# Kernel tuning notes

Measured on AMD Instinct MI355X. Metric: run time of the kernel, lower is better.

Reference implementation:

```python
import jax, jax.numpy as jnp
import numpy as np

B, TX, TS = 64, 2048, 10
D, L, NMELS, MAXR, R = 256, 1024, 80, 20, 2


def gru_cell(x, h, wih, whh, bih, bhh):
    # torch GRUCell: gates ordered (r, z, n)
    gi = x @ wih.T + bih
    gh = h @ whh.T + bhh
    ir, iz, inn = jnp.split(gi, 3, axis=-1)
    hr, hz, hn = jnp.split(gh, 3, axis=-1)
    r = jax.nn.sigmoid(ir + hr)
    z = jax.nn.sigmoid(iz + hz)
    n = jnp.tanh(inn + r * hn)
    return (1.0 - z) * n + z * h


def lstm_cell(x, h, c, wih, whh, bih, bhh):
    # torch LSTMCell: gates ordered (i, f, g, o)
    g = x @ wih.T + bih + h @ whh.T + bhh
    i, f, gg, o = jnp.split(g, 4, axis=-1)
    c_new = jax.nn.sigmoid(f) * c + jax.nn.sigmoid(i) * jnp.tanh(gg)
    h_new = jax.nn.sigmoid(o) * jnp.tanh(c_new)
    return h_new, c_new


def attention(enc, query, W, v):
    # u = v @ tanh(enc + W q); softmax over time
    qp = query @ W.T                                  # [B, D]
    u = jnp.tanh(enc + qp[:, None, :]) @ v            # [B, T]
    scores = jax.nn.softmax(u, axis=-1)               # [B, T]
    ctx = jnp.einsum('bt,btd->bd', scores, enc)       # [B, D]
    return scores, ctx


def setup_inputs() -> dict:
    key = jax.random.key(0)
    ks = jax.random.split(key, 40)
    n = lambda i, shape, s=0.02: jax.random.normal(ks[i], shape, dtype=jnp.float32) * s
    return {
        'encoder_seq': n(0, (B, TX, D), 1.0),
        'style_embed': n(1, (B, TS, D), 1.0),
        'prenet_in': n(2, (B, NMELS), 1.0),
        'h_text': n(3, (B, D), 1.0), 'h_style': n(4, (B, D), 1.0), 'h_attn': n(5, (B, D), 1.0),
        'h_r1': n(6, (B, L), 1.0), 'h_r2': n(7, (B, L), 1.0),
        'c_r1': n(8, (B, L), 1.0), 'c_r2': n(9, (B, L), 1.0),
        'cv_text': n(10, (B, D), 1.0), 'cv_style': n(11, (B, D), 1.0), 'cv': n(12, (B, D), 1.0),
        'fc1_w': n(13, (256, NMELS)), 'fc1_b': jnp.zeros((256,), jnp.float32),
        'fc2_w': n(14, (128, 256)), 'fc2_b': jnp.zeros((128,), jnp.float32),
        'tW': n(15, (D, D)), 'tv': n(16, (D,)),
        'sW': n(17, (D, D)), 'sv': n(18, (D,)),
        't_wih': n(19, (3 * D, D + 128)), 't_whh': n(20, (3 * D, D)),
        't_bih': jnp.zeros((3 * D,), jnp.float32), 't_bhh': jnp.zeros((3 * D,), jnp.float32),
        's_wih': n(21, (3 * D, D + 128)), 's_whh': n(22, (3 * D, D)),
        's_bih': jnp.zeros((3 * D,), jnp.float32), 's_bhh': jnp.zeros((3 * D,), jnp.float32),
        'a_wih': n(23, (3 * D, D + 128)), 'a_whh': n(24, (3 * D, D)),
        'a_bih': jnp.zeros((3 * D,), jnp.float32), 'a_bhh': jnp.zeros((3 * D,), jnp.float32),
        'ri_w': n(25, (L, 2 * D)), 'ri_b': jnp.zeros((L,), jnp.float32),
        'l1_wih': n(26, (4 * L, L)), 'l1_whh': n(27, (4 * L, L)),
        'l1_bih': jnp.zeros((4 * L,), jnp.float32), 'l1_bhh': jnp.zeros((4 * L,), jnp.float32),
        'l2_wih': n(28, (4 * L, L)), 'l2_whh': n(29, (4 * L, L)),
        'l2_bih': jnp.zeros((4 * L,), jnp.float32), 'l2_bhh': jnp.zeros((4 * L,), jnp.float32),
        'mp_w': n(30, (NMELS * MAXR, L)),
        't': 0,
    }


def reference(encoder_seq, style_embed, prenet_in, h_text, h_style, h_attn,
              h_r1, h_r2, c_r1, c_r2, cv_text, cv_style, cv,
              fc1_w, fc1_b, fc2_w, fc2_b, tW, tv, sW, sv,
              t_wih, t_whh, t_bih, t_bhh, s_wih, s_whh, s_bih, s_bhh,
              a_wih, a_whh, a_bih, a_bhh, ri_w, ri_b,
              l1_wih, l1_whh, l1_bih, l1_bhh, l2_wih, l2_whh, l2_bih, l2_bhh,
              mp_w, t):
    # PreNet (eval mode: no dropout)
    p = jax.nn.relu(prenet_in @ fc1_w.T + fc1_b)
    p = jax.nn.relu(p @ fc2_w.T + fc2_b)                      # [B, 128]

    text_in = jnp.concatenate([cv_text, p], axis=-1)          # [B, D+128]
    style_in = jnp.concatenate([cv_style, p], axis=-1)
    attn_in = jnp.concatenate([cv, p], axis=-1)

    h_text = gru_cell(text_in, h_text, t_wih, t_whh, t_bih, t_bhh)
    text_scores, cv_text = attention(encoder_seq, h_text, tW, tv)

    h_style = gru_cell(style_in, h_style, s_wih, s_whh, s_bih, s_bhh)
    style_scores, cv_style = attention(style_embed, h_style, sW, sv)

    cv_new = cv_text                                          # context_vec = text_context_vec
    h_attn = gru_cell(attn_in, h_attn, a_wih, a_whh, a_bih, a_bhh)

    x = jnp.concatenate([cv_new, h_attn], axis=1) @ ri_w.T + ri_b  # [B, L]
    h_r1, c_r1 = lstm_cell(x, h_r1, c_r1, l1_wih, l1_whh, l1_bih, l1_bhh)
    x = x + h_r1
    h_r2, c_r2 = lstm_cell(x, h_r2, c_r2, l2_wih, l2_whh, l2_bih, l2_bhh)
    x = x + h_r2

    mels = (x @ mp_w.T).reshape(B, NMELS, MAXR)[:, :, :R]     # [B, n_mels, r]
    return mels
```

## Files before the change

### kernel.cpp

```cpp
#include <hip/hip_runtime.h>
#include <hip/hip_bf16.h>

typedef unsigned short u16;
typedef unsigned int   u32;
typedef __attribute__((ext_vector_type(8))) short bf16x8;
typedef __attribute__((ext_vector_type(4))) float f32x4;

#define NB   64
#define NTX  2048
#define ND   256
#define NL   1024

#if __has_builtin(__builtin_amdgcn_exp2f)
#define EXP2F(x) __builtin_amdgcn_exp2f(x)
#else
#define EXP2F(x) exp2f(x)
#endif
#if __has_builtin(__builtin_amdgcn_rcpf)
#define RCPF(x) __builtin_amdgcn_rcpf(x)
#else
#define RCPF(x) (1.0f/(x))
#endif

__device__ __forceinline__ u16 f2bf(float f){
  union { float f; u32 u; } c; c.f = f;
  return (u16)((c.u + 0x7fffu + ((c.u >> 16) & 1u)) >> 16);
}
__device__ __forceinline__ u32 pk2(float a, float b){
  return (u32)f2bf(a) | ((u32)f2bf(b) << 16);
}
__device__ __forceinline__ float sigmf(float x){ return 1.f/(1.f+__expf(-x)); }
__device__ __forceinline__ float tanhf_fast(float x){
  x = fminf(fmaxf(x, -15.f), 15.f);
  float e = __expf(2.f*x);
  return (e - 1.f) / (e + 1.f);
}
__device__ __forceinline__ float dot_rowf(const float* __restrict__ row,
                                          const float* __restrict__ x, int K4){
  float acc = 0.f;
  for (int j = 0; j < K4; ++j){
    float4 w = *(const float4*)(row + j*4);
    const float* xp = x + j*4;
    acc += w.x*xp[0] + w.y*xp[1] + w.z*xp[2] + w.w*xp[3];
  }
  return acc;
}

__global__ __launch_bounds__(256) void k_pre1(
    const float* __restrict__ cv_text, const float* __restrict__ cv,
    const float* __restrict__ h_text,  const float* __restrict__ h_attn,
    const float* __restrict__ prenet_in,
    const float* __restrict__ fc1_w, const float* __restrict__ fc1_b,
    const float* __restrict__ h_r1, const float* __restrict__ h_r2,
    float* __restrict__ xtext, float* __restrict__ xattn,
    float* __restrict__ htT,  float* __restrict__ haT,
    float* __restrict__ p1T,
    u16* __restrict__ hb1, u16* __restrict__ hb2)
{
  __shared__ float ld[64][65];
  const int blk = blockIdx.x, tid = threadIdx.x;
  if (blk < 16){
    int a = blk >> 2; int c0 = (blk & 3)*64;
    const float* src = (a==0)?cv_text:(a==1)?cv:(a==2)?h_text:h_attn;
    float* dst = (a==0)?xtext:(a==1)?xattn:(a==2)?htT:haT;
    const int r = tid >> 2, q = tid & 3;
    #pragma unroll
    for (int i = 0; i < 4; ++i){
      float4 v = *(const float4*)(src + (size_t)r*256 + c0 + q*16 + i*4);
      ld[r][q*16+i*4+0] = v.x; ld[r][q*16+i*4+1] = v.y;
      ld[r][q*16+i*4+2] = v.z; ld[r][q*16+i*4+3] = v.w;
    }
    __syncthreads();
    const int cc = tid >> 2;
    #pragma unroll
    for (int i = 0; i < 4; ++i){
      int b0 = q*16 + i*4;
      float4 o = { ld[b0+0][cc], ld[b0+1][cc], ld[b0+2][cc], ld[b0+3][cc] };
      *(float4*)(dst + (size_t)(c0+cc)*64 + b0) = o;
    }
  } else if (blk < 80){
    const int wave = tid >> 6, lane = tid & 63;
    const int n = (blk - 16)*4 + wave;
    float acc = fc1_b[n];
    const float* wr = fc1_w + (size_t)n*80;
    const float* xr = prenet_in + (size_t)lane*80;
    #pragma unroll
    for (int k = 0; k < 80; k += 4){
      float4 w = *(const float4*)(wr + k);
      acc += w.x*xr[k] + w.y*xr[k+1] + w.z*xr[k+2] + w.w*xr[k+3];
    }
    p1T[n*64 + lane] = fmaxf(acc, 0.f);
  } else {
    const int t2 = blk - 80;
    const float* src = (t2 < 32) ? h_r1 : h_r2;
    u16* dst = (t2 < 32) ? hb1 : hb2;
    const int base = (t2 & 31)*2048 + tid*8;
    float4 a = *(const float4*)(src + base);
    float4 b = *(const float4*)(src + base + 4);
    uint4 o = { pk2(a.x,a.y), pk2(a.z,a.w), pk2(b.x,b.y), pk2(b.z,b.w) };
    *(uint4*)(dst + base) = o;
  }
}

__global__ __launch_bounds__(256) void k_pre2(
    const float* __restrict__ p1T,
    const float* __restrict__ fc2_w, const float* __restrict__ fc2_b,
    float* __restrict__ xtext, float* __restrict__ xattn)
{
  const int tid = threadIdx.x, w = tid >> 6, lane = tid & 63;
  const int n = blockIdx.x;
  __shared__ float red[4][64];
  float acc = 0.f;
  const float* wr = fc2_w + (size_t)n*256 + w*64;
  const float* xb = p1T + w*64*64 + lane;
  #pragma unroll
  for (int k = 0; k < 64; k += 4){
    float4 wv = *(const float4*)(wr + k);
    acc += wv.x*xb[(k+0)*64] + wv.y*xb[(k+1)*64]
         + wv.z*xb[(k+2)*64] + wv.w*xb[(k+3)*64];
  }
  red[w][lane] = acc;
  __syncthreads();
  if (w == 0){
    float v = fmaxf(red[0][lane]+red[1][lane]+red[2][lane]+red[3][lane] + fc2_b[n], 0.f);
    xtext[(size_t)(256+n)*64 + lane] = v;
    xattn[(size_t)(256+n)*64 + lane] = v;
  }
}

__global__ __launch_bounds__(512) void k_gru(
    const float* __restrict__ t_wih, const float* __restrict__ t_whh,
    const float* __restrict__ t_bih, const float* __restrict__ t_bhh,
    const float* __restrict__ a_wih, const float* __restrict__ a_whh,
    const float* __restrict__ a_bih, const float* __restrict__ a_bhh,
    const float* __restrict__ xtext, const float* __restrict__ xattn,
    const float* __restrict__ htT,  const float* __restrict__ haT,
    float* __restrict__ htnT, u16* __restrict__ xrib)
{
  const int tid = threadIdx.x, w = tid >> 6, lane = tid & 63;
  const int isA = blockIdx.x >= 256;
  const int d = blockIdx.x & 255;
  const float* wih = isA ? a_wih : t_wih;
  const float* whh = isA ? a_whh : t_whh;
  const float* xT  = isA ? xattn : xtext;
  const float* hT  = isA ? haT   : htT;
  __shared__ float red[8][6][64];
  float s0=0.f,s1=0.f,s2=0.f,s3=0.f,s4=0.f,s5=0.f;
  {
    const float* wr = wih + (size_t)d*384       + w*48;
    const float* wz = wih + (size_t)(256+d)*384 + w*48;
    const float* wn = wih + (size_t)(512+d)*384 + w*48;
    const float* xb = xT + w*48*64 + lane;
    #pragma unroll 4
    for (int k = 0; k < 48; k += 4){
      float4 ar = *(const float4*)(wr + k);
      float4 az = *(const float4*)(wz + k);
      float4 an = *(const float4*)(wn + k);
      float x0 = xb[(k+0)*64], x1 = xb[(k+1)*64];
      float x2 = xb[(k+2)*64], x3 = xb[(k+3)*64];
      s0 += ar.x*x0 + ar.y*x1 + ar.z*x2 + ar.w*x3;
      s1 += az.x*x0 + az.y*x1 + az.z*x2 + az.w*x3;
      s2 += an.x*x0 + an.y*x1 + an.z*x2 + an.w*x3;
    }
  }
  {
    const float* vr = whh + (size_t)d*256       + w*32;
    const float* vz = whh + (size_t)(256+d)*256 + w*32;
    const float* vn = whh + (size_t)(512+d)*256 + w*32;
    const float* hb = hT + w*32*64 + lane;
    #pragma unroll 4
    for (int k = 0; k < 32; k += 4){
      float4 ar = *(const float4*)(vr + k);
      float4 az = *(const float4*)(vz + k);
      float4 an = *(const float4*)(vn + k);
      float h0 = hb[(k+0)*64], h1 = hb[(k+1)*64];
      float h2 = hb[(k+2)*64], h3 = hb[(k+3)*64];
      s3 += ar.x*h0 + ar.y*h1 + ar.z*h2 + ar.w*h3;
      s4 += az.x*h0 + az.y*h1 + az.z*h2 + az.w*h3;
      s5 += an.x*h0 + an.y*h1 + an.z*h2 + an.w*h3;
    }
  }
  red[w][0][lane]=s0; red[w][1][lane]=s1; red[w][2][lane]=s2;
  red[w][3][lane]=s3; red[w][4][lane]=s4; red[w][5][lane]=s5;
  __syncthreads();
  if (w == 0){
    const float* bih = isA ? a_bih : t_bih;
    const float* bhh = isA ? a_bhh : t_bhh;
    float g6[6];
    #pragma unroll
    for (int i = 0; i < 6; ++i){
      float a = 0.f;
      #pragma unroll
      for (int ww = 0; ww < 8; ++ww) a += red[ww][i][lane];
      g6[i] = a;
    }
    float gir = bih[d]     + g6[0];
    float giz = bih[256+d] + g6[1];
    float gin = bih[512+d] + g6[2];
    float ghr = bhh[d]     + g6[3];
    float ghz = bhh[256+d] + g6[4];
    float ghn = bhh[512+d] + g6[5];
    float hd = hT[d*64 + lane];
    float r  = sigmf(gir + ghr), z = sigmf(giz + ghz);
    float nn = tanhf_fast(gin + r*ghn);
    float hnew = (1.f - z)*nn + z*hd;
    if (isA) xrib[(size_t)lane*512 + 256 + d] = f2bf(hnew);
    else     htnT[(size_t)d*64 + lane]        = hnew;
  }
}

__global__ __launch_bounds__(256) void k_qp(
    const float* __restrict__ tWm, const float* __restrict__ htnT,
    float* __restrict__ qp)
{
  const int tid = threadIdx.x, w = tid >> 6, lane = tid & 63;
  const int d = blockIdx.x;
  __shared__ float red[4][64];
  float acc = 0.f;
  const float* wr = tWm + (size_t)d*256 + w*64;
  const float* xb = htnT + w*64*64 + lane;
  #pragma unroll
  for (int k = 0; k < 64; k += 4){
    float4 wv = *(const float4*)(wr + k);
    acc += wv.x*xb[(k+0)*64] + wv.y*xb[(k+1)*64]
         + wv.z*xb[(k+2)*64] + wv.w*xb[(k+3)*64];
  }
  red[w][lane] = acc;
  __syncthreads();
  if (w == 0)
    qp[lane*ND + d] = red[0][lane]+red[1][lane]+red[2][lane]+red[3][lane];
}

__global__ __launch_bounds__(256) void k_attn_part(
    const float* __restrict__ enc, const float* __restrict__ qp,
    const float* __restrict__ tv,  float* __restrict__ attnP)
{
  const int tid = threadIdx.x, b = blockIdx.x, ch = blockIdx.y;
  const int wave = tid >> 6, lane = tid & 63;
  const float C2  = 2.885390082f;
  const float L2E = 1.4426950408f;
  __shared__ float qpL[256], vL[256], ctxL[4][256], sL[4];
  qpL[tid] = qp[b*ND + tid] * C2;
  vL[tid]  = tv[tid] * 2.f;
  __syncthreads();

  const float q0 = qpL[lane*4+0], q1 = qpL[lane*4+1], q2 = qpL[lane*4+2], q3 = qpL[lane*4+3];
  const float v0 = vL[lane*4+0],  v1 = vL[lane*4+1],  v2 = vL[lane*4+2],  v3 = vL[lane*4+3];
  float vs = 0.5f*(v0 + v1 + v2 + v3);
  #pragma unroll
  for (int off = 1; off < 64; off <<= 1) vs += __shfl_xor(vs, off);
  const float VS = vs;

  float cx0=0.f, cx1=0.f, cx2=0.f, cx3=0.f, sacc=0.f;
  const float* base = enc + ((size_t)b*NTX + (size_t)ch*128 + wave*32)*ND + lane*4;
  #pragma unroll 4
  for (int i = 0; i < 32; ++i){
    float4 ev = *(const float4*)(base + (size_t)i*ND);
    float e0 = ev.x, e1 = ev.y, e2 = ev.z, e3 = ev.w;
    float srow;
    {
      float u0 = EXP2F(__builtin_fmaf(e0, C2, q0));
      float u1 = EXP2F(__builtin_fmaf(e1, C2, q1));
      float u2 = EXP2F(__builtin_fmaf(e2, C2, q2));
      float u3 = EXP2F(__builtin_fmaf(e3, C2, q3));
      srow = v0*RCPF(u0 + 1.f) + v1*RCPF(u1 + 1.f)
           + v2*RCPF(u2 + 1.f) + v3*RCPF(u3 + 1.f);
    }
    #pragma unroll
    for (int off = 1; off < 64; off <<= 1) srow += __shfl_xor(srow, off);
    float w = EXP2F((VS - srow) * L2E);
    sacc += w;
    cx0 = __builtin_fmaf(w, e0, cx0); cx1 = __builtin_fmaf(w, e1, cx1);
    cx2 = __builtin_fmaf(w, e2, cx2); cx3 = __builtin_fmaf(w, e3, cx3);
  }
  ctxL[wave][lane*4+0]=cx0; ctxL[wave][lane*4+1]=cx1;
  ctxL[wave][lane*4+2]=cx2; ctxL[wave][lane*4+3]=cx3;
  if (lane == 0) sL[wave] = sacc;
  __syncthreads();
  float c = ctxL[0][tid]+ctxL[1][tid]+ctxL[2][tid]+ctxL[3][tid];
  float* dst = attnP + ((size_t)b*16 + ch)*257;
  dst[tid] = c;
  if (tid == 0) dst[256] = sL[0]+sL[1]+sL[2]+sL[3];
}

__global__ __launch_bounds__(256) void k_attn_red(
    const float* __restrict__ attnP, u16* __restrict__ xrib)
{
  const int tid = threadIdx.x, b = blockIdx.x;
  float c = 0.f, s = 0.f;
  for (int ch = 0; ch < 16; ++ch){
    const float* src = attnP + ((size_t)b*16 + ch)*257;
    c += src[tid]; s += src[256];
  }
  xrib[(size_t)b*512 + tid] = f2bf(c / s);
}


__global__ __launch_bounds__(512) void k_mm_ri(
    const u16* __restrict__ xrib, const float* __restrict__ ri_w,
    const float* __restrict__ ri_b, float* __restrict__ x0,
    u16* __restrict__ x0b)
{
  __shared__ float Rs[8][4][4][65];
  const int tid = threadIdx.x, lane = tid & 63, w = tid >> 6;
  const int n0 = blockIdx.x * 16;
  f32x4 acc[4];
  #pragma unroll
  for (int i = 0; i < 4; ++i) acc[i] = (f32x4){0.f,0.f,0.f,0.f};
  const int kbase = w*64;
  const float* wr = ri_w + (size_t)(n0 + (lane & 15))*512 + kbase + (lane >> 4)*8;
  const u16* xs = xrib + (size_t)(lane & 15)*512 + kbase + (lane >> 4)*8;
  #pragma unroll
  for (int t = 0; t < 2; ++t){
    float4 wa = *(const float4*)(wr + t*32);
    float4 wb = *(const float4*)(wr + t*32 + 4);
    union { bf16x8 v; uint4 u; } bf;
    bf.u.x = pk2(wa.x,wa.y); bf.u.y = pk2(wa.z,wa.w);
    bf.u.z = pk2(wb.x,wb.y); bf.u.w = pk2(wb.z,wb.w);
    #pragma unroll
    for (int fb = 0; fb < 4; ++fb){
      union { bf16x8 v; uint4 u; } af;
      af.u = *(const uint4*)(xs + fb*16*512 + t*32);
      acc[fb] = __builtin_amdgcn_mfma_f32_16x16x32_bf16(af.v, bf.v, acc[fb], 0, 0, 0);
    }
  }
  #pragma unroll
  for (int fb = 0; fb < 4; ++fb)
    #pragma unroll
    for (int r = 0; r < 4; ++r) Rs[w][fb][r][lane] = acc[fb][r];
  __syncthreads();
  if (tid < 256){
    const int b = tid >> 2, c4 = (tid & 3)*4;
    const int fb = b >> 4, q = (b >> 2) & 3, reg = b & 3;
    #pragma unroll
    for (int cc = 0; cc < 4; ++cc){
      const int c = c4 + cc;
      float v = ri_b[n0 + c];
      #pragma unroll
      for (int ww = 0; ww < 8; ++ww) v += Rs[ww][fb][reg][q*16 + c];
      x0[(size_t)b*1024 + n0 + c]  = v;
      x0b[(size_t)b*1024 + n0 + c] = f2bf(v);
    }
  }
}

__global__ __launch_bounds__(1024) void k_lstm(
    const float* __restrict__ Wih, const float* __restrict__ Whh,
    const u16* __restrict__ xb, const u16* __restrict__ hb,
    const float* __restrict__ bih, const float* __restrict__ bhh,
    const float* __restrict__ c_in,
    const float* __restrict__ xin, float* __restrict__ xout,
    u16* __restrict__ xoutb)
{
  __shared__ float Rs[16][4][4][65];
  const int tid = threadIdx.x, lane = tid & 63, w = tid >> 6;
  const int j0 = blockIdx.x * 4;
  const float* W = (w < 8) ? Wih : Whh;
  const u16*   X = (w < 8) ? xb  : hb;
  const int kbase = (w & 7) * 128;

  f32x4 acc[4];
  #pragma unroll
  for (int i = 0; i < 4; ++i) acc[i] = (f32x4){0.f,0.f,0.f,0.f};
  const int r16 = lane & 15;
  const int g = r16 >> 2, jq = r16 & 3;
  const float* wr = W + (size_t)(g*1024 + j0 + jq)*1024 + kbase + (lane >> 4)*8;
  #pragma unroll
  for (int t = 0; t < 4; ++t){
    float4 wa = *(const float4*)(wr + t*32);
    float4 wb = *(const float4*)(wr + t*32 + 4);
    union { bf16x8 v; uint4 u; } bf;
    bf.u.x = pk2(wa.x,wa.y); bf.u.y = pk2(wa.z,wa.w);
    bf.u.z = pk2(wb.x,wb.y); bf.u.w = pk2(wb.z,wb.w);
    #pragma unroll
    for (int fb = 0; fb < 4; ++fb){
      union { bf16x8 v; uint4 u; } af;
      af.u = *(const uint4*)(X + (size_t)(fb*16 + r16)*1024 + kbase + (lane >> 4)*8 + t*32);
      acc[fb] = __builtin_amdgcn_mfma_f32_16x16x32_bf16(af.v, bf.v, acc[fb], 0, 0, 0);
    }
  }
  #pragma unroll
  for (int fb = 0; fb < 4; ++fb)
    #pragma unroll
    for (int r = 0; r < 4; ++r) Rs[w][fb][r][lane] = acc[fb][r];
  __syncthreads();

  if (tid < 256){
    const int b  = tid >> 2, jq2 = tid & 3;
    const int j  = j0 + jq2;
    const int fb = b >> 4, q = (b >> 2) & 3, reg = b & 3;
    float gate[4];
    #pragma unroll
    for (int gg = 0; gg < 4; ++gg){
      const int li = q*16 + gg*4 + jq2;
      float a = bih[gg*1024 + j] + bhh[gg*1024 + j];
      #pragma unroll
      for (int ww = 0; ww < 16; ++ww) a += Rs[ww][fb][reg][li];
      gate[gg] = a;
    }
    float ii = sigmf(gate[0]), ff = sigmf(gate[1]);
    float gv = tanhf_fast(gate[2]), oo = sigmf(gate[3]);
    float cc = ff * c_in[(size_t)b*1024 + j] + ii * gv;
    float hh = oo * tanhf_fast(cc);
    float xo = xin[(size_t)b*1024 + j] + hh;
    xout[(size_t)b*1024 + j]  = xo;
    xoutb[(size_t)b*1024 + j] = f2bf(xo);
  }
}

__global__ __launch_bounds__(256) void k_mels(
    const float* __restrict__ x2, const float* __restrict__ mp_w,
    float* __restrict__ out)
{
  const int tid = threadIdx.x, b = blockIdx.x;
  __shared__ float xL[NL];
  #pragma unroll
  for (int i = 0; i < 4; ++i){
    int j = tid + 256*i;
    xL[j] = x2[(size_t)b*NL + j];
  }
  __syncthreads();
  if (tid < 160){
    int m = tid >> 1, r = tid & 1;
    float acc = dot_rowf(mp_w + (size_t)(m*20 + r)*NL, xL, 256);
    out[b*160 + tid] = acc;
  }
}

extern "C" void kernel_launch(void* const* d_in, const int* in_sizes, int n_in,
                              void* d_out, int out_size, void* d_ws, size_t ws_size,
                              hipStream_t stream)
{
  (void)in_sizes; (void)n_in; (void)out_size; (void)ws_size;
  const float* enc     = (const float*)d_in[0];
  const float* pre_in  = (const float*)d_in[2];
  const float* h_text  = (const float*)d_in[3];
  const float* h_attn  = (const float*)d_in[5];
  const float* h_r1    = (const float*)d_in[6];
  const float* h_r2    = (const float*)d_in[7];
  const float* c_r1    = (const float*)d_in[8];
  const float* c_r2    = (const float*)d_in[9];
  const float* cv_text = (const float*)d_in[10];
  const float* cv      = (const float*)d_in[12];
  const float* fc1_w   = (const float*)d_in[13];
  const float* fc1_b   = (const float*)d_in[14];
  const float* fc2_w   = (const float*)d_in[15];
  const float* fc2_b   = (const float*)d_in[16];
  const float* tWm     = (const float*)d_in[17];
  const float* tv      = (const float*)d_in[18];
  const float* t_wih   = (const float*)d_in[21];
  const float* t_whh   = (const float*)d_in[22];
  const float* t_bih   = (const float*)d_in[23];
  const float* t_bhh   = (const float*)d_in[24];
  const float* a_wih   = (const float*)d_in[29];
  const float* a_whh   = (const float*)d_in[30];
  const float* a_bih   = (const float*)d_in[31];
  const float* a_bhh   = (const float*)d_in[32];
  const float* ri_w    = (const float*)d_in[33];
  const float* ri_b    = (const float*)d_in[34];
  const float* l1_wih  = (const float*)d_in[35];
  const float* l1_whh  = (const float*)d_in[36];
  const float* l1_bih  = (const float*)d_in[37];
  const float* l1_bhh  = (const float*)d_in[38];
  const float* l2_wih  = (const float*)d_in[39];
  const float* l2_whh  = (const float*)d_in[40];
  const float* l2_bih  = (const float*)d_in[41];
  const float* l2_bhh  = (const float*)d_in[42];
  const float* mp_w    = (const float*)d_in[43];

  float* ws    = (float*)d_ws;
  float* qp    = ws;
  float* attnP = qp    + 16384;
  float* x0    = attnP + 263168;
  float* x1    = x0    + 65536;
  float* x2    = x1    + 65536;
  float* xtext = x2    + 65536;
  float* xattn = xtext + 24576;
  float* htT   = xattn + 24576;
  float* haT   = htT   + 16384;
  float* htnT  = haT   + 16384;
  float* p1T   = htnT  + 16384;
  u16*   hb1   = (u16*)(p1T + 16384);
  u16*   hb2   = hb1 + 65536;
  u16*   xrib  = hb2 + 65536;
  u16*   x0b   = xrib + 32768;
  u16*   x1b   = x0b + 65536;
  u16*   x2b   = x1b + 65536;

  k_pre1<<<144, 256, 0, stream>>>(cv_text, cv, h_text, h_attn,
      pre_in, fc1_w, fc1_b, h_r1, h_r2,
      xtext, xattn, htT, haT, p1T, hb1, hb2);
  k_pre2<<<128, 256, 0, stream>>>(p1T, fc2_w, fc2_b, xtext, xattn);
  k_gru<<<512, 512, 0, stream>>>(t_wih, t_whh, t_bih, t_bhh,
      a_wih, a_whh, a_bih, a_bhh, xtext, xattn, htT, haT, htnT, xrib);
  k_qp<<<256, 256, 0, stream>>>(tWm, htnT, qp);

  k_attn_part<<<dim3(64,16), 256, 0, stream>>>(enc, qp, tv, attnP);
  k_attn_red<<<64, 256, 0, stream>>>(attnP, xrib);

  k_mm_ri<<<64, 512, 0, stream>>>(xrib, ri_w, ri_b, x0, x0b);

  k_lstm<<<256, 1024, 0, stream>>>(l1_wih, l1_whh, x0b, hb1,
      l1_bih, l1_bhh, c_r1, x0, x1, x1b);
  k_lstm<<<256, 1024, 0, stream>>>(l2_wih, l2_whh, x1b, hb2,
      l2_bih, l2_bhh, c_r2, x1, x2, x2b);

  k_mels<<<64, 256, 0, stream>>>(x2, mp_w, (float*)d_out);
}
```

Measured before the change: 115.6 us.

## Fuse all decoder stages into one cooperative persistent kernel with grid syncs

Replaces the chain of ten small kernel launches with a single cooperative kernel of 256 blocks × 1024 threads. Stages are separated by grid.sync() and mapped onto virtual sub-blocks. The point is to remove launch gaps and per-kernel ramp-up on a tiny, latency-bound step. It also reshapes the attention split (fewer partials, the attnP workspace shrinks) and folds the context normalization into the ri matmul stage, and it skews the shared-memory reduction indices to avoid bank conflicts. In exchange, every stage now runs at a fixed 1024-thread occupancy, and each grid barrier has its own cost.

```diff
diff --git a/kernel.cpp b/kernel.cpp
--- a/kernel.cpp
+++ b/kernel.cpp
@@ -1,5 +1,8 @@
 #include <hip/hip_runtime.h>
+#include <hip/hip_cooperative_groups.h>
 #include <hip/hip_bf16.h>
+
+namespace cg = cooperative_groups;
 
 typedef unsigned short u16;
 typedef unsigned int   u32;
@@ -35,330 +38,32 @@
   float e = __expf(2.f*x);
   return (e - 1.f) / (e + 1.f);
 }
-__device__ __forceinline__ float dot_rowf(const float* __restrict__ row,
-                                          const float* __restrict__ x, int K4){
-  float acc = 0.f;
-  for (int j = 0; j < K4; ++j){
-    float4 w = *(const float4*)(row + j*4);
-    const float* xp = x + j*4;
-    acc += w.x*xp[0] + w.y*xp[1] + w.z*xp[2] + w.w*xp[3];
-  }
-  return acc;
-}
-
-__global__ __launch_bounds__(256) void k_pre1(
-    const float* __restrict__ cv_text, const float* __restrict__ cv,
-    const float* __restrict__ h_text,  const float* __restrict__ h_attn,
-    const float* __restrict__ prenet_in,
-    const float* __restrict__ fc1_w, const float* __restrict__ fc1_b,
-    const float* __restrict__ h_r1, const float* __restrict__ h_r2,
-    float* __restrict__ xtext, float* __restrict__ xattn,
-    float* __restrict__ htT,  float* __restrict__ haT,
-    float* __restrict__ p1T,
-    u16* __restrict__ hb1, u16* __restrict__ hb2)
-{
-  __shared__ float ld[64][65];
-  const int blk = blockIdx.x, tid = threadIdx.x;
-  if (blk < 16){
-    int a = blk >> 2; int c0 = (blk & 3)*64;
-    const float* src = (a==0)?cv_text:(a==1)?cv:(a==2)?h_text:h_attn;
-    float* dst = (a==0)?xtext:(a==1)?xattn:(a==2)?htT:haT;
-    const int r = tid >> 2, q = tid & 3;
-    #pragma unroll
-    for (int i = 0; i < 4; ++i){
-      float4 v = *(const float4*)(src + (size_t)r*256 + c0 + q*16 + i*4);
-      ld[r][q*16+i*4+0] = v.x; ld[r][q*16+i*4+1] = v.y;
-      ld[r][q*16+i*4+2] = v.z; ld[r][q*16+i*4+3] = v.w;
-    }
-    __syncthreads();
-    const int cc = tid >> 2;
-    #pragma unroll
-    for (int i = 0; i < 4; ++i){
-      int b0 = q*16 + i*4;
-      float4 o = { ld[b0+0][cc], ld[b0+1][cc], ld[b0+2][cc], ld[b0+3][cc] };
-      *(float4*)(dst + (size_t)(c0+cc)*64 + b0) = o;
-    }
-  } else if (blk < 80){
-    const int wave = tid >> 6, lane = tid & 63;
-    const int n = (blk - 16)*4 + wave;
-    float acc = fc1_b[n];
-    const float* wr = fc1_w + (size_t)n*80;
-    const float* xr = prenet_in + (size_t)lane*80;
-    #pragma unroll
-    for (int k = 0; k < 80; k += 4){
-      float4 w = *(const float4*)(wr + k);
-      acc += w.x*xr[k] + w.y*xr[k+1] + w.z*xr[k+2] + w.w*xr[k+3];
-    }
-    p1T[n*64 + lane] = fmaxf(acc, 0.f);
-  } else {
-    const int t2 = blk - 80;
-    const float* src = (t2 < 32) ? h_r1 : h_r2;
-    u16* dst = (t2 < 32) ? hb1 : hb2;
-    const int base = (t2 & 31)*2048 + tid*8;
-    float4 a = *(const float4*)(src + base);
-    float4 b = *(const float4*)(src + base + 4);
-    uint4 o = { pk2(a.x,a.y), pk2(a.z,a.w), pk2(b.x,b.y), pk2(b.z,b.w) };
-    *(uint4*)(dst + base) = o;
-  }
-}
-
-__global__ __launch_bounds__(256) void k_pre2(
-    const float* __restrict__ p1T,
-    const float* __restrict__ fc2_w, const float* __restrict__ fc2_b,
-    float* __restrict__ xtext, float* __restrict__ xattn)
-{
-  const int tid = threadIdx.x, w = tid >> 6, lane = tid & 63;
-  const int n = blockIdx.x;
-  __shared__ float red[4][64];
-  float acc = 0.f;
-  const float* wr = fc2_w + (size_t)n*256 + w*64;
-  const float* xb = p1T + w*64*64 + lane;
-  #pragma unroll
-  for (int k = 0; k < 64; k += 4){
-    float4 wv = *(const float4*)(wr + k);
-    acc += wv.x*xb[(k+0)*64] + wv.y*xb[(k+1)*64]
-         + wv.z*xb[(k+2)*64] + wv.w*xb[(k+3)*64];
-  }
-  red[w][lane] = acc;
-  __syncthreads();
-  if (w == 0){
-    float v = fmaxf(red[0][lane]+red[1][lane]+red[2][lane]+red[3][lane] + fc2_b[n], 0.f);
-    xtext[(size_t)(256+n)*64 + lane] = v;
-    xattn[(size_t)(256+n)*64 + lane] = v;
-  }
-}
-
-__global__ __launch_bounds__(512) void k_gru(
-    const float* __restrict__ t_wih, const float* __restrict__ t_whh,
-    const float* __restrict__ t_bih, const float* __restrict__ t_bhh,
-    const float* __restrict__ a_wih, const float* __restrict__ a_whh,
-    const float* __restrict__ a_bih, const float* __restrict__ a_bhh,
-    const float* __restrict__ xtext, const float* __restrict__ xattn,
-    const float* __restrict__ htT,  const float* __restrict__ haT,
-    float* __restrict__ htnT, u16* __restrict__ xrib)
-{
-  const int tid = threadIdx.x, w = tid >> 6, lane = tid & 63;
-  const int isA = blockIdx.x >= 256;
-  const int d = blockIdx.x & 255;
-  const float* wih = isA ? a_wih : t_wih;
-  const float* whh = isA ? a_whh : t_whh;
-  const float* xT  = isA ? xattn : xtext;
-  const float* hT  = isA ? haT   : htT;
-  __shared__ float red[8][6][64];
-  float s0=0.f,s1=0.f,s2=0.f,s3=0.f,s4=0.f,s5=0.f;
-  {
-    const float* wr = wih + (size_t)d*384       + w*48;
-    const float* wz = wih + (size_t)(256+d)*384 + w*48;
-    const float* wn = wih + (size_t)(512+d)*384 + w*48;
-    const float* xb = xT + w*48*64 + lane;
-    #pragma unroll 4
-    for (int k = 0; k < 48; k += 4){
-      float4 ar = *(const float4*)(wr + k);
-      float4 az = *(const float4*)(wz + k);
-      float4 an = *(const float4*)(wn + k);
-      float x0 = xb[(k+0)*64], x1 = xb[(k+1)*64];
-      float x2 = xb[(k+2)*64], x3 = xb[(k+3)*64];
-      s0 += ar.x*x0 + ar.y*x1 + ar.z*x2 + ar.w*x3;
-      s1 += az.x*x0 + az.y*x1 + az.z*x2 + az.w*x3;
-      s2 += an.x*x0 + an.y*x1 + an.z*x2 + an.w*x3;
-    }
-  }
-  {
-    const float* vr = whh + (size_t)d*256       + w*32;
-    const float* vz = whh + (size_t)(256+d)*256 + w*32;
-    const float* vn = whh + (size_t)(512+d)*256 + w*32;
-    const float* hb = hT + w*32*64 + lane;
-    #pragma unroll 4
-    for (int k = 0; k < 32; k += 4){
-      float4 ar = *(const float4*)(vr + k);
-      float4 az = *(const float4*)(vz + k);
-      float4 an = *(const float4*)(vn + k);
-      float h0 = hb[(k+0)*64], h1 = hb[(k+1)*64];
-      float h2 = hb[(k+2)*64], h3 = hb[(k+3)*64];
-      s3 += ar.x*h0 + ar.y*h1 + ar.z*h2 + ar.w*h3;
-      s4 += az.x*h0 + az.y*h1 + az.z*h2 + az.w*h3;
-      s5 += an.x*h0 + an.y*h1 + an.z*h2 + an.w*h3;
-    }
-  }
-  red[w][0][lane]=s0; red[w][1][lane]=s1; red[w][2][lane]=s2;
-  red[w][3][lane]=s3; red[w][4][lane]=s4; red[w][5][lane]=s5;
-  __syncthreads();
-  if (w == 0){
-    const float* bih = isA ? a_bih : t_bih;
-    const float* bhh = isA ? a_bhh : t_bhh;
-    float g6[6];
-    #pragma unroll
-    for (int i = 0; i < 6; ++i){
-      float a = 0.f;
-      #pragma unroll
-      for (int ww = 0; ww < 8; ++ww) a += red[ww][i][lane];
-      g6[i] = a;
-    }
-    float gir = bih[d]     + g6[0];
-    float giz = bih[256+d] + g6[1];
-    float gin = bih[512+d] + g6[2];
-    float ghr = bhh[d]     + g6[3];
-    float ghz = bhh[256+d] + g6[4];
-    float ghn = bhh[512+d] + g6[5];
-    float hd = hT[d*64 + lane];
-    float r  = sigmf(gir + ghr), z = sigmf(giz + ghz);
-    float nn = tanhf_fast(gin + r*ghn);
-    float hnew = (1.f - z)*nn + z*hd;
-    if (isA) xrib[(size_t)lane*512 + 256 + d] = f2bf(hnew);
-    else     htnT[(size_t)d*64 + lane]        = hnew;
-  }
-}
-
-__global__ __launch_bounds__(256) void k_qp(
-    const float* __restrict__ tWm, const float* __restrict__ htnT,
-    float* __restrict__ qp)
-{
-  const int tid = threadIdx.x, w = tid >> 6, lane = tid & 63;
-  const int d = blockIdx.x;
-  __shared__ float red[4][64];
-  float acc = 0.f;
-  const float* wr = tWm + (size_t)d*256 + w*64;
-  const float* xb = htnT + w*64*64 + lane;
-  #pragma unroll
-  for (int k = 0; k < 64; k += 4){
-    float4 wv = *(const float4*)(wr + k);
-    acc += wv.x*xb[(k+0)*64] + wv.y*xb[(k+1)*64]
-         + wv.z*xb[(k+2)*64] + wv.w*xb[(k+3)*64];
-  }
-  red[w][lane] = acc;
-  __syncthreads();
-  if (w == 0)
-    qp[lane*ND + d] = red[0][lane]+red[1][lane]+red[2][lane]+red[3][lane];
-}
-
-__global__ __launch_bounds__(256) void k_attn_part(
-    const float* __restrict__ enc, const float* __restrict__ qp,
-    const float* __restrict__ tv,  float* __restrict__ attnP)
-{
-  const int tid = threadIdx.x, b = blockIdx.x, ch = blockIdx.y;
-  const int wave = tid >> 6, lane = tid & 63;
-  const float C2  = 2.885390082f;
-  const float L2E = 1.4426950408f;
-  __shared__ float qpL[256], vL[256], ctxL[4][256], sL[4];
-  qpL[tid] = qp[b*ND + tid] * C2;
-  vL[tid]  = tv[tid] * 2.f;
-  __syncthreads();
-
-  const float q0 = qpL[lane*4+0], q1 = qpL[lane*4+1], q2 = qpL[lane*4+2], q3 = qpL[lane*4+3];
-  const float v0 = vL[lane*4+0],  v1 = vL[lane*4+1],  v2 = vL[lane*4+2],  v3 = vL[lane*4+3];
-  float vs = 0.5f*(v0 + v1 + v2 + v3);
-  #pragma unroll
-  for (int off = 1; off < 64; off <<= 1) vs += __shfl_xor(vs, off);
-  const float VS = vs;
-
-  float cx0=0.f, cx1=0.f, cx2=0.f, cx3=0.f, sacc=0.f;
-  const float* base = enc + ((size_t)b*NTX + (size_t)ch*128 + wave*32)*ND + lane*4;
-  #pragma unroll 4
-  for (int i = 0; i < 32; ++i){
-    float4 ev = *(const float4*)(base + (size_t)i*ND);
-    float e0 = ev.x, e1 = ev.y, e2 = ev.z, e3 = ev.w;
-    float srow;
-    {
-      float u0 = EXP2F(__builtin_fmaf(e0, C2, q0));
-      float u1 = EXP2F(__builtin_fmaf(e1, C2, q1));
-      float u2 = EXP2F(__builtin_fmaf(e2, C2, q2));
-      float u3 = EXP2F(__builtin_fmaf(e3, C2, q3));
-      srow = v0*RCPF(u0 + 1.f) + v1*RCPF(u1 + 1.f)
-           + v2*RCPF(u2 + 1.f) + v3*RCPF(u3 + 1.f);
-    }
-    #pragma unroll
-    for (int off = 1; off < 64; off <<= 1) srow += __shfl_xor(srow, off);
-    float w = EXP2F((VS - srow) * L2E);
-    sacc += w;
-    cx0 = __builtin_fmaf(w, e0, cx0); cx1 = __builtin_fmaf(w, e1, cx1);
-    cx2 = __builtin_fmaf(w, e2, cx2); cx3 = __builtin_fmaf(w, e3, cx3);
-  }
-  ctxL[wave][lane*4+0]=cx0; ctxL[wave][lane*4+1]=cx1;
-  ctxL[wave][lane*4+2]=cx2; ctxL[wave][lane*4+3]=cx3;
-  if (lane == 0) sL[wave] = sacc;
-  __syncthreads();
-  float c = ctxL[0][tid]+ctxL[1][tid]+ctxL[2][tid]+ctxL[3][tid];
-  float* dst = attnP + ((size_t)b*16 + ch)*257;
-  dst[tid] = c;
-  if (tid == 0) dst[256] = sL[0]+sL[1]+sL[2]+sL[3];
-}
-
-__global__ __launch_bounds__(256) void k_attn_red(
-    const float* __restrict__ attnP, u16* __restrict__ xrib)
-{
-  const int tid = threadIdx.x, b = blockIdx.x;
-  float c = 0.f, s = 0.f;
-  for (int ch = 0; ch < 16; ++ch){
-    const float* src = attnP + ((size_t)b*16 + ch)*257;
-    c += src[tid]; s += src[256];
-  }
-  xrib[(size_t)b*512 + tid] = f2bf(c / s);
-}
-
-
-__global__ __launch_bounds__(512) void k_mm_ri(
-    const u16* __restrict__ xrib, const float* __restrict__ ri_w,
-    const float* __restrict__ ri_b, float* __restrict__ x0,
-    u16* __restrict__ x0b)
-{
-  __shared__ float Rs[8][4][4][65];
-  const int tid = threadIdx.x, lane = tid & 63, w = tid >> 6;
-  const int n0 = blockIdx.x * 16;
-  f32x4 acc[4];
-  #pragma unroll
-  for (int i = 0; i < 4; ++i) acc[i] = (f32x4){0.f,0.f,0.f,0.f};
-  const int kbase = w*64;
-  const float* wr = ri_w + (size_t)(n0 + (lane & 15))*512 + kbase + (lane >> 4)*8;
-  const u16* xs = xrib + (size_t)(lane & 15)*512 + kbase + (lane >> 4)*8;
-  #pragma unroll
-  for (int t = 0; t < 2; ++t){
-    float4 wa = *(const float4*)(wr + t*32);
-    float4 wb = *(const float4*)(wr + t*32 + 4);
-    union { bf16x8 v; uint4 u; } bf;
-    bf.u.x = pk2(wa.x,wa.y); bf.u.y = pk2(wa.z,wa.w);
-    bf.u.z = pk2(wb.x,wb.y); bf.u.w = pk2(wb.z,wb.w);
-    #pragma unroll
-    for (int fb = 0; fb < 4; ++fb){
-      union { bf16x8 v; uint4 u; } af;
-      af.u = *(const uint4*)(xs + fb*16*512 + t*32);
-      acc[fb] = __builtin_amdgcn_mfma_f32_16x16x32_bf16(af.v, bf.v, acc[fb], 0, 0, 0);
-    }
-  }
-  #pragma unroll
-  for (int fb = 0; fb < 4; ++fb)
-    #pragma unroll
-    for (int r = 0; r < 4; ++r) Rs[w][fb][r][lane] = acc[fb][r];
-  __syncthreads();
-  if (tid < 256){
-    const int b = tid >> 2, c4 = (tid & 3)*4;
-    const int fb = b >> 4, q = (b >> 2) & 3, reg = b & 3;
-    #pragma unroll
-    for (int cc = 0; cc < 4; ++cc){
-      const int c = c4 + cc;
-      float v = ri_b[n0 + c];
-      #pragma unroll
-      for (int ww = 0; ww < 8; ++ww) v += Rs[ww][fb][reg][q*16 + c];
-      x0[(size_t)b*1024 + n0 + c]  = v;
-      x0b[(size_t)b*1024 + n0 + c] = f2bf(v);
-    }
-  }
-}
-
-__global__ __launch_bounds__(1024) void k_lstm(
+
+struct MA {
+  const float *enc, *pre_in, *h_r1, *h_r2, *c_r1, *c_r2,
+              *cv_text, *cv, *h_text, *h_attn,
+              *fc1_w, *fc1_b, *fc2_w, *fc2_b, *tWm, *tv,
+              *t_wih, *t_whh, *t_bih, *t_bhh,
+              *a_wih, *a_whh, *a_bih, *a_bhh,
+              *ri_w, *ri_b, *l1_wih, *l1_whh, *l1_bih, *l1_bhh,
+              *l2_wih, *l2_whh, *l2_bih, *l2_bhh, *mp_w;
+  float *qp, *attnP, *x0, *x1, *x2, *xtext, *xattn, *htT, *haT, *htnT, *p1T;
+  u16 *hb1, *hb2, *xrib, *x0b, *x1b, *x2b;
+  float* out;
+};
+
+__device__ __forceinline__ void lstm_stage(const MA& a, float* Rs,
     const float* __restrict__ Wih, const float* __restrict__ Whh,
     const u16* __restrict__ xb, const u16* __restrict__ hb,
     const float* __restrict__ bih, const float* __restrict__ bhh,
-    const float* __restrict__ c_in,
-    const float* __restrict__ xin, float* __restrict__ xout,
-    u16* __restrict__ xoutb)
+    const float* __restrict__ c_in, const float* __restrict__ xin,
+    float* __restrict__ xout, u16* __restrict__ xoutb)
 {
-  __shared__ float Rs[16][4][4][65];
   const int tid = threadIdx.x, lane = tid & 63, w = tid >> 6;
   const int j0 = blockIdx.x * 4;
   const float* W = (w < 8) ? Wih : Whh;
   const u16*   X = (w < 8) ? xb  : hb;
   const int kbase = (w & 7) * 128;
-
   f32x4 acc[4];
   #pragma unroll
   for (int i = 0; i < 4; ++i) acc[i] = (f32x4){0.f,0.f,0.f,0.f};
@@ -382,9 +87,9 @@
   #pragma unroll
   for (int fb = 0; fb < 4; ++fb)
     #pragma unroll
-    for (int r = 0; r < 4; ++r) Rs[w][fb][r][lane] = acc[fb][r];
+    for (int r = 0; r < 4; ++r)
+      Rs[w*1024 + fb*256 + r*64 + ((lane + w*4) & 63)] = acc[fb][r];
   __syncthreads();
-
   if (tid < 256){
     const int b  = tid >> 2, jq2 = tid & 3;
     const int j  = j0 + jq2;
@@ -393,10 +98,11 @@
     #pragma unroll
     for (int gg = 0; gg < 4; ++gg){
       const int li = q*16 + gg*4 + jq2;
-      float a = bih[gg*1024 + j] + bhh[gg*1024 + j];
-      #pragma unroll
-      for (int ww = 0; ww < 16; ++ww) a += Rs[ww][fb][reg][li];
-      gate[gg] = a;
+      float s = bih[gg*1024 + j] + bhh[gg*1024 + j];
+      #pragma unroll
+      for (int ww = 0; ww < 16; ++ww)
+        s += Rs[ww*1024 + fb*256 + reg*64 + ((li + ww*4) & 63)];
+      gate[gg] = s;
     }
     float ii = sigmf(gate[0]), ff = sigmf(gate[1]);
     float gv = tanhf_fast(gate[2]), oo = sigmf(gate[3]);
@@ -408,22 +114,318 @@
   }
 }
 
-__global__ __launch_bounds__(256) void k_mels(
-    const float* __restrict__ x2, const float* __restrict__ mp_w,
-    float* __restrict__ out)
+__global__ __launch_bounds__(1024) void k_mega(MA a)
 {
-  const int tid = threadIdx.x, b = blockIdx.x;
-  __shared__ float xL[NL];
-  #pragma unroll
-  for (int i = 0; i < 4; ++i){
-    int j = tid + 256*i;
-    xL[j] = x2[(size_t)b*NL + j];
-  }
-  __syncthreads();
-  if (tid < 160){
-    int m = tid >> 1, r = tid & 1;
-    float acc = dot_rowf(mp_w + (size_t)(m*20 + r)*NL, xL, 256);
-    out[b*160 + tid] = acc;
+  __shared__ char smem[65536];
+  float* smemf = (float*)smem;
+  cg::grid_group grid = cg::this_grid();
+  const int tid = threadIdx.x, blk = blockIdx.x;
+  const int lane = tid & 63, w = tid >> 6;
+  const int vblk = blk*4 + (tid >> 8), vtid = tid & 255;
+
+  if (vblk < 16){
+    int ai = vblk >> 2, c0 = (vblk & 3)*64;
+    const float* src = (ai==0)?a.cv_text:(ai==1)?a.cv:(ai==2)?a.h_text:a.h_attn;
+    float* dst = (ai==0)?a.xtext:(ai==1)?a.xattn:(ai==2)?a.htT:a.haT;
+    const int b = vtid & 63, cq = vtid >> 6;
+    #pragma unroll
+    for (int i = 0; i < 16; ++i){
+      int c = c0 + cq + i*4;
+      dst[(size_t)c*64 + b] = src[(size_t)b*256 + c];
+    }
+  } else if (vblk < 80){
+    const int wv = vtid >> 6, ln = vtid & 63;
+    const int n = (vblk - 16)*4 + wv;
+    float acc = a.fc1_b[n];
+    const float* wr = a.fc1_w + (size_t)n*80;
+    const float* xr = a.pre_in + (size_t)ln*80;
+    #pragma unroll
+    for (int k = 0; k < 80; k += 4){
+      float4 wq = *(const float4*)(wr + k);
+      acc += wq.x*xr[k] + wq.y*xr[k+1] + wq.z*xr[k+2] + wq.w*xr[k+3];
+    }
+    a.p1T[n*64 + ln] = fmaxf(acc, 0.f);
+  } else if (vblk < 144){
+    const int t2 = vblk - 80;
+    const float* src = (t2 < 32) ? a.h_r1 : a.h_r2;
+    u16* dst = (t2 < 32) ? a.hb1 : a.hb2;
+    const int base = (t2 & 31)*2048 + vtid*8;
+    float4 p = *(const float4*)(src + base);
+    float4 q = *(const float4*)(src + base + 4);
+    uint4 o = { pk2(p.x,p.y), pk2(p.z,p.w), pk2(q.x,q.y), pk2(q.z,q.w) };
+    *(uint4*)(dst + base) = o;
+  }
+  grid.sync();
+
+  if (blk < 32){
+    const int n = vblk;
+    const int wv = vtid >> 6, ln = vtid & 63;
+    float* red = smemf + (tid >> 8)*256;
+    float acc = 0.f;
+    const float* wr = a.fc2_w + (size_t)n*256 + wv*64;
+    const float* xb = a.p1T + wv*64*64 + ln;
+    #pragma unroll
+    for (int k = 0; k < 64; k += 4){
+      float4 wq = *(const float4*)(wr + k);
+      acc += wq.x*xb[(k+0)*64] + wq.y*xb[(k+1)*64]
+           + wq.z*xb[(k+2)*64] + wq.w*xb[(k+3)*64];
+    }
+    red[wv*64 + ln] = acc;
+    __syncthreads();
+    if (wv == 0){
+      float v = fmaxf(red[ln]+red[64+ln]+red[128+ln]+red[192+ln] + a.fc2_b[n], 0.f);
+      a.xtext[(size_t)(256+n)*64 + ln] = v;
+      a.xattn[(size_t)(256+n)*64 + ln] = v;
+    }
+  }
+  grid.sync();
+
+  {
+    const int d = blk;
+    const int isA = (w >= 8), w8 = w & 7;
+    const float* wih = isA ? a.a_wih : a.t_wih;
+    const float* whh = isA ? a.a_whh : a.t_whh;
+    const float* xT  = isA ? a.xattn : a.xtext;
+    const float* hT  = isA ? a.haT   : a.htT;
+    float* red = smemf;
+    float s0=0.f,s1=0.f,s2=0.f,s3=0.f,s4=0.f,s5=0.f;
+    {
+      const float* wr = wih + (size_t)d*384       + w8*48;
+      const float* wz = wih + (size_t)(256+d)*384 + w8*48;
+      const float* wn = wih + (size_t)(512+d)*384 + w8*48;
+      const float* xb = xT + w8*48*64 + lane;
+      #pragma unroll 4
+      for (int k = 0; k < 48; k += 4){
+        float4 ar = *(const float4*)(wr + k);
+        float4 az = *(const float4*)(wz + k);
+        float4 an = *(const float4*)(wn + k);
+        float x0 = xb[(k+0)*64], x1 = xb[(k+1)*64];
+        float x2 = xb[(k+2)*64], x3 = xb[(k+3)*64];
+        s0 += ar.x*x0 + ar.y*x1 + ar.z*x2 + ar.w*x3;
+        s1 += az.x*x0 + az.y*x1 + az.z*x2 + az.w*x3;
+        s2 += an.x*x0 + an.y*x1 + an.z*x2 + an.w*x3;
+      }
+    }
+    {
+      const float* vr = whh + (size_t)d*256       + w8*32;
+      const float* vz = whh + (size_t)(256+d)*256 + w8*32;
+      const float* vn = whh + (size_t)(512+d)*256 + w8*32;
+      const float* hb = hT + w8*32*64 + lane;
+      #pragma unroll 4
+      for (int k = 0; k < 32; k += 4){
+        float4 ar = *(const float4*)(vr + k);
+        float4 az = *(const float4*)(vz + k);
+        float4 an = *(const float4*)(vn + k);
+        float h0 = hb[(k+0)*64], h1 = hb[(k+1)*64];
+        float h2 = hb[(k+2)*64], h3 = hb[(k+3)*64];
+        s3 += ar.x*h0 + ar.y*h1 + ar.z*h2 + ar.w*h3;
+        s4 += az.x*h0 + az.y*h1 + az.z*h2 + az.w*h3;
+        s5 += an.x*h0 + an.y*h1 + an.z*h2 + an.w*h3;
+      }
+    }
+    red[(w*6+0)*64+lane]=s0; red[(w*6+1)*64+lane]=s1; red[(w*6+2)*64+lane]=s2;
+    red[(w*6+3)*64+lane]=s3; red[(w*6+4)*64+lane]=s4; red[(w*6+5)*64+lane]=s5;
+    __syncthreads();
+    if (w == 0 || w == 8){
+      const int base = (w == 8) ? 8 : 0;
+      const float* bih = (w==8) ? a.a_bih : a.t_bih;
+      const float* bhh = (w==8) ? a.a_bhh : a.t_bhh;
+      const float* hT2 = (w==8) ? a.haT   : a.htT;
+      float g6[6];
+      #pragma unroll
+      for (int i = 0; i < 6; ++i){
+        float s = 0.f;
+        #pragma unroll
+        for (int ww = 0; ww < 8; ++ww) s += red[((base+ww)*6+i)*64 + lane];
+        g6[i] = s;
+      }
+      float gir = bih[d]     + g6[0];
+      float giz = bih[256+d] + g6[1];
+      float gin = bih[512+d] + g6[2];
+      float ghr = bhh[d]     + g6[3];
+      float ghz = bhh[256+d] + g6[4];
+      float ghn = bhh[512+d] + g6[5];
+      float hd = hT2[d*64 + lane];
+      float r  = sigmf(gir + ghr), z = sigmf(giz + ghz);
+      float nn = tanhf_fast(gin + r*ghn);
+      float hnew = (1.f - z)*nn + z*hd;
+      if (w == 8) a.xrib[(size_t)lane*512 + 256 + d] = f2bf(hnew);
+      else        a.htnT[(size_t)d*64 + lane]        = hnew;
+    }
+  }
+  grid.sync();
+
+  if (blk < 64){
+    const int d = vblk;
+    const int wv = vtid >> 6, ln = vtid & 63;
+    float* red = smemf + (tid >> 8)*256;
+    float acc = 0.f;
+    const float* wr = a.tWm + (size_t)d*256 + wv*64;
+    const float* xb = a.htnT + wv*64*64 + ln;
+    #pragma unroll
+    for (int k = 0; k < 64; k += 4){
+      float4 wq = *(const float4*)(wr + k);
+      acc += wq.x*xb[(k+0)*64] + wq.y*xb[(k+1)*64]
+           + wq.z*xb[(k+2)*64] + wq.w*xb[(k+3)*64];
+    }
+    red[wv*64 + ln] = acc;
+    __syncthreads();
+    if (wv == 0)
+      a.qp[ln*ND + d] = red[ln]+red[64+ln]+red[128+ln]+red[192+ln];
+  }
+  grid.sync();
+
+  {
+    const int b = blk >> 2, chg = blk & 3;
+    const float C2  = 2.885390082f;
+    const float L2E = 1.4426950408f;
+    float* qpL  = smemf;
+    float* vL   = smemf + 256;
+    float* ctxL = smemf + 512;
+    float* sL   = smemf + 512 + 4096;
+    if (tid < 256){
+      qpL[tid] = a.qp[b*ND + tid] * C2;
+      vL[tid]  = a.tv[tid] * 2.f;
+    }
+    __syncthreads();
+    const float q0 = qpL[lane*4+0], q1 = qpL[lane*4+1], q2 = qpL[lane*4+2], q3 = qpL[lane*4+3];
+    const float v0 = vL[lane*4+0],  v1 = vL[lane*4+1],  v2 = vL[lane*4+2],  v3 = vL[lane*4+3];
+    float vs = 0.5f*(v0 + v1 + v2 + v3);
+    #pragma unroll
+    for (int off = 1; off < 64; off <<= 1) vs += __shfl_xor(vs, off);
+    const float VS = vs;
+    float cx0=0.f, cx1=0.f, cx2=0.f, cx3=0.f, sacc=0.f;
+    const float* base = a.enc + ((size_t)b*NTX + (size_t)chg*512 + w*32)*ND + lane*4;
+    #pragma unroll 4
+    for (int i = 0; i < 32; ++i){
+      float4 ev = *(const float4*)(base + (size_t)i*ND);
+      float e0 = ev.x, e1 = ev.y, e2 = ev.z, e3 = ev.w;
+      float u0 = EXP2F(__builtin_fmaf(e0, C2, q0));
+      float u1 = EXP2F(__builtin_fmaf(e1, C2, q1));
+      float u2 = EXP2F(__builtin_fmaf(e2, C2, q2));
+      float u3 = EXP2F(__builtin_fmaf(e3, C2, q3));
+      float srow = v0*RCPF(u0 + 1.f) + v1*RCPF(u1 + 1.f)
+                 + v2*RCPF(u2 + 1.f) + v3*RCPF(u3 + 1.f);
+      #pragma unroll
+      for (int off = 1; off < 64; off <<= 1) srow += __shfl_xor(srow, off);
+      float ww = EXP2F((VS - srow) * L2E);
+      sacc += ww;
+      cx0 = __builtin_fmaf(ww, e0, cx0); cx1 = __builtin_fmaf(ww, e1, cx1);
+      cx2 = __builtin_fmaf(ww, e2, cx2); cx3 = __builtin_fmaf(ww, e3, cx3);
+    }
+    ctxL[w*256 + lane*4+0]=cx0; ctxL[w*256 + lane*4+1]=cx1;
+    ctxL[w*256 + lane*4+2]=cx2; ctxL[w*256 + lane*4+3]=cx3;
+    if (lane == 0) sL[w] = sacc;
+    __syncthreads();
+    if (tid < 256){
+      float c = 0.f;
+      #pragma unroll
+      for (int ww = 0; ww < 16; ++ww) c += ctxL[ww*256 + tid];
+      a.attnP[(size_t)blk*257 + tid] = c;
+      if (tid == 0){
+        float s = 0.f;
+        #pragma unroll
+        for (int ww = 0; ww < 16; ++ww) s += sL[ww];
+        a.attnP[(size_t)blk*257 + 256] = s;
+      }
+    }
+  }
+  grid.sync();
+
+  if (blk < 64){
+    u16*   xctxb = (u16*)smem;
+    float* Rs    = (float*)(smem + 32768);
+    {
+      const int b = tid >> 4, cg16 = tid & 15;
+      float s = a.attnP[(size_t)(b*4+0)*257 + 256] + a.attnP[(size_t)(b*4+1)*257 + 256]
+              + a.attnP[(size_t)(b*4+2)*257 + 256] + a.attnP[(size_t)(b*4+3)*257 + 256];
+      float inv = RCPF(s);
+      #pragma unroll
+      for (int i = 0; i < 16; ++i){
+        int c = cg16*16 + i;
+        float v = a.attnP[(size_t)(b*4+0)*257 + c] + a.attnP[(size_t)(b*4+1)*257 + c]
+                + a.attnP[(size_t)(b*4+2)*257 + c] + a.attnP[(size_t)(b*4+3)*257 + c];
+        xctxb[b*256 + c] = f2bf(v * inv);
+      }
+    }
+    __syncthreads();
+    const int n0 = blk * 16;
+    if (w < 8){
+      f32x4 acc[4];
+      #pragma unroll
+      for (int i = 0; i < 4; ++i) acc[i] = (f32x4){0.f,0.f,0.f,0.f};
+      const int kbase = w*64;
+      const float* wr = a.ri_w + (size_t)(n0 + (lane & 15))*512 + kbase + (lane >> 4)*8;
+      #pragma unroll
+      for (int t = 0; t < 2; ++t){
+        float4 wa = *(const float4*)(wr + t*32);
+        float4 wb = *(const float4*)(wr + t*32 + 4);
+        union { bf16x8 v; uint4 u; } bf;
+        bf.u.x = pk2(wa.x,wa.y); bf.u.y = pk2(wa.z,wa.w);
+        bf.u.z = pk2(wb.x,wb.y); bf.u.w = pk2(wb.z,wb.w);
+        #pragma unroll
+        for (int fb = 0; fb < 4; ++fb){
+          union { bf16x8 v; uint4 u; } af;
+          const int row = fb*16 + (lane & 15);
+          if (w < 4)
+            af.u = *(const uint4*)(xctxb + row*256 + kbase + (lane >> 4)*8 + t*32);
+          else
+            af.u = *(const uint4*)(a.xrib + (size_t)row*512 + kbase + (lane >> 4)*8 + t*32);
+          acc[fb] = __builtin_amdgcn_mfma_f32_16x16x32_bf16(af.v, bf.v, acc[fb], 0, 0, 0);
+        }
+      }
+      #pragma unroll
+      for (int fb = 0; fb < 4; ++fb)
+        #pragma unroll
+        for (int r = 0; r < 4; ++r)
+          Rs[w*1024 + fb*256 + r*64 + ((lane + w*4) & 63)] = acc[fb][r];
+    }
+    __syncthreads();
+    if (tid < 256){
+      const int b = tid >> 2, c4 = (tid & 3)*4;
+      const int fb = b >> 4, q = (b >> 2) & 3, reg = b & 3;
+      #pragma unroll
+      for (int cc = 0; cc < 4; ++cc){
+        const int c = c4 + cc;
+        const int li = q*16 + c;
+        float v = a.ri_b[n0 + c];
+        #pragma unroll
+        for (int ww = 0; ww < 8; ++ww)
+          v += Rs[ww*1024 + fb*256 + reg*64 + ((li + ww*4) & 63)];
+        a.x0[(size_t)b*1024 + n0 + c]  = v;
+        a.x0b[(size_t)b*1024 + n0 + c] = f2bf(v);
+      }
+    }
+  }
+  grid.sync();
+
+  lstm_stage(a, smemf, a.l1_wih, a.l1_whh, a.x0b, a.hb1,
+             a.l1_bih, a.l1_bhh, a.c_r1, a.x0, a.x1, a.x1b);
+  grid.sync();
+
+  lstm_stage(a, smemf, a.l2_wih, a.l2_whh, a.x1b, a.hb2,
+             a.l2_bih, a.l2_bhh, a.c_r2, a.x1, a.x2, a.x2b);
+  grid.sync();
+
+  if (blk < 16){
+    const int b = vblk;
+    float* xL = smemf + (tid >> 8)*1024;
+    #pragma unroll
+    for (int i = 0; i < 4; ++i){
+      int j = vtid + 256*i;
+      xL[j] = a.x2[(size_t)b*NL + j];
+    }
+    __syncthreads();
+    if (vtid < 160){
+      int m = vtid >> 1, r = vtid & 1;
+      const float* row = a.mp_w + (size_t)(m*20 + r)*NL;
+      float acc = 0.f;
+      for (int k = 0; k < 1024; k += 4){
+        float4 wq = *(const float4*)(row + k);
+        acc += wq.x*xL[k] + wq.y*xL[k+1] + wq.z*xL[k+2] + wq.w*xL[k+3];
+      }
+      a.out[b*160 + vtid] = acc;
+    }
   }
 }
 
@@ -432,78 +434,64 @@
                               hipStream_t stream)
 {
   (void)in_sizes; (void)n_in; (void)out_size; (void)ws_size;
-  const float* enc     = (const float*)d_in[0];
-  const float* pre_in  = (const float*)d_in[2];
-  const float* h_text  = (const float*)d_in[3];
-  const float* h_attn  = (const float*)d_in[5];
-  const float* h_r1    = (const float*)d_in[6];
-  const float* h_r2    = (const float*)d_in[7];
-  const float* c_r1    = (const float*)d_in[8];
-  const float* c_r2    = (const float*)d_in[9];
-  const float* cv_text = (const float*)d_in[10];
-  const float* cv      = (const float*)d_in[12];
-  const float* fc1_w   = (const float*)d_in[13];
-  const float* fc1_b   = (const float*)d_in[14];
-  const float* fc2_w   = (const float*)d_in[15];
-  const float* fc2_b   = (const float*)d_in[16];
-  const float* tWm     = (const float*)d_in[17];
-  const float* tv      = (const float*)d_in[18];
-  const float* t_wih   = (const float*)d_in[21];
-  const float* t_whh   = (const float*)d_in[22];
-  const float* t_bih   = (const float*)d_in[23];
-  const float* t_bhh   = (const float*)d_in[24];
-  const float* a_wih   = (const float*)d_in[29];
-  const float* a_whh   = (const float*)d_in[30];
-  const float* a_bih   = (const float*)d_in[31];
-  const float* a_bhh   = (const float*)d_in[32];
-  const float* ri_w    = (const float*)d_in[33];
-  const float* ri_b    = (const float*)d_in[34];
-  const float* l1_wih  = (const float*)d_in[35];
-  const float* l1_whh  = (const float*)d_in[36];
-  const float* l1_bih  = (const float*)d_in[37];
-  const float* l1_bhh  = (const float*)d_in[38];
-  const float* l2_wih  = (const float*)d_in[39];
-  const float* l2_whh  = (const float*)d_in[40];
-  const float* l2_bih  = (const float*)d_in[41];
-  const float* l2_bhh  = (const float*)d_in[42];
-  const float* mp_w    = (const float*)d_in[43];
-
-  float* ws    = (float*)d_ws;
-  float* qp    = ws;
-  float* attnP = qp    + 16384;
-  float* x0    = attnP + 263168;
-  float* x1    = x0    + 65536;
-  float* x2    = x1    + 65536;
-  float* xtext = x2    + 65536;
-  float* xattn = xtext + 24576;
-  float* htT   = xattn + 24576;
-  float* haT   = htT   + 16384;
-  float* htnT  = haT   + 16384;
-  float* p1T   = htnT  + 16384;
-  u16*   hb1   = (u16*)(p1T + 16384);
-  u16*   hb2   = hb1 + 65536;
-  u16*   xrib  = hb2 + 65536;
-  u16*   x0b   = xrib + 32768;
-  u16*   x1b   = x0b + 65536;
-  u16*   x2b   = x1b + 65536;
-
-  k_pre1<<<144, 256, 0, stream>>>(cv_text, cv, h_text, h_attn,
-      pre_in, fc1_w, fc1_b, h_r1, h_r2,
-      xtext, xattn, htT, haT, p1T, hb1, hb2);
-  k_pre2<<<128, 256, 0, stream>>>(p1T, fc2_w, fc2_b, xtext, xattn);
-  k_gru<<<512, 512, 0, stream>>>(t_wih, t_whh, t_bih, t_bhh,
-      a_wih, a_whh, a_bih, a_bhh, xtext, xattn, htT, haT, htnT, xrib);
-  k_qp<<<256, 256, 0, stream>>>(tWm, htnT, qp);
-
-  k_attn_part<<<dim3(64,16), 256, 0, stream>>>(enc, qp, tv, attnP);
-  k_attn_red<<<64, 256, 0, stream>>>(attnP, xrib);
-
-  k_mm_ri<<<64, 512, 0, stream>>>(xrib, ri_w, ri_b, x0, x0b);
-
-  k_lstm<<<256, 1024, 0, stream>>>(l1_wih, l1_whh, x0b, hb1,
-      l1_bih, l1_bhh, c_r1, x0, x1, x1b);
-  k_lstm<<<256, 1024, 0, stream>>>(l2_wih, l2_whh, x1b, hb2,
-      l2_bih, l2_bhh, c_r2, x1, x2, x2b);
-
-  k_mels<<<64, 256, 0, stream>>>(x2, mp_w, (float*)d_out);
-}
+  MA a;
+  a.enc     = (const float*)d_in[0];
+  a.pre_in  = (const float*)d_in[2];
+  a.h_text  = (const float*)d_in[3];
+  a.h_attn  = (const float*)d_in[5];
+  a.h_r1    = (const float*)d_in[6];
+  a.h_r2    = (const float*)d_in[7];
+  a.c_r1    = (const float*)d_in[8];
+  a.c_r2    = (const float*)d_in[9];
+  a.cv_text = (const float*)d_in[10];
+  a.cv      = (const float*)d_in[12];
+  a.fc1_w   = (const float*)d_in[13];
+  a.fc1_b   = (const float*)d_in[14];
+  a.fc2_w   = (const float*)d_in[15];
+  a.fc2_b   = (const float*)d_in[16];
+  a.tWm     = (const float*)d_in[17];
+  a.tv      = (const float*)d_in[18];
+  a.t_wih   = (const float*)d_in[21];
+  a.t_whh   = (const float*)d_in[22];
+  a.t_bih   = (const float*)d_in[23];
+  a.t_bhh   = (const float*)d_in[24];
+  a.a_wih   = (const float*)d_in[29];
+  a.a_whh   = (const float*)d_in[30];
+  a.a_bih   = (const float*)d_in[31];
+  a.a_bhh   = (const float*)d_in[32];
+  a.ri_w    = (const float*)d_in[33];
+  a.ri_b    = (const float*)d_in[34];
+  a.l1_wih  = (const float*)d_in[35];
+  a.l1_whh  = (const float*)d_in[36];
+  a.l1_bih  = (const float*)d_in[37];
+  a.l1_bhh  = (const float*)d_in[38];
+  a.l2_wih  = (const float*)d_in[39];
+  a.l2_whh  = (const float*)d_in[40];
+  a.l2_bih  = (const float*)d_in[41];
+  a.l2_bhh  = (const float*)d_in[42];
+  a.mp_w    = (const float*)d_in[43];
+
+  float* ws = (float*)d_ws;
+  a.qp    = ws;
+  a.attnP = a.qp    + 16384;
+  a.x0    = a.attnP + 65792;
+  a.x1    = a.x0    + 65536;
+  a.x2    = a.x1    + 65536;
+  a.xtext = a.x2    + 65536;
+  a.xattn = a.xtext + 24576;
+  a.htT   = a.xattn + 24576;
+  a.haT   = a.htT   + 16384;
+  a.htnT  = a.haT   + 16384;
+  a.p1T   = a.htnT  + 16384;
+  a.hb1   = (u16*)(a.p1T + 16384);
+  a.hb2   = a.hb1 + 65536;
+  a.xrib  = a.hb2 + 65536;
+  a.x0b   = a.xrib + 32768;
+  a.x1b   = a.x0b + 65536;
+  a.x2b   = a.x1b + 65536;
+  a.out   = (float*)d_out;
+
+  void* args[] = { &a };
+  hipLaunchCooperativeKernel((const void*)k_mega, dim3(256), dim3(1024),
+                             args, 0, stream);
+}
```

Result: slower. 392.3 us (+239.4%).
